# Optimization experiments

Measured on AMD Instinct MI355X. Metric: run time of the kernel, lower is better.

The kernel has to match this reference:

```python
import jax, jax.numpy as jnp
import numpy as np

VOCAB = 50000
B, T, D_OUT = 32, 512, 256
E_DIMS = (300, 300, 200)


def setup_inputs() -> dict:
    key = jax.random.key(0)
    ks = jax.random.split(key, 8)
    ids = jax.random.randint(ks[0], (B, T), 0, VOCAB)
    E0 = jax.random.normal(ks[1], (VOCAB, E_DIMS[0]), dtype=jnp.float32)
    E1 = jax.random.normal(ks[2], (VOCAB, E_DIMS[1]), dtype=jnp.float32)
    E2 = jax.random.normal(ks[3], (VOCAB, E_DIMS[2]), dtype=jnp.float32)
    # Glorot-ish scaled projection weights
    W0 = jax.random.normal(ks[4], (E_DIMS[0], D_OUT), dtype=jnp.float32) / np.sqrt(E_DIMS[0])
    W1 = jax.random.normal(ks[5], (E_DIMS[1], D_OUT), dtype=jnp.float32) / np.sqrt(E_DIMS[1])
    W2 = jax.random.normal(ks[6], (E_DIMS[2], D_OUT), dtype=jnp.float32) / np.sqrt(E_DIMS[2])
    Wa = jax.random.normal(ks[7], (D_OUT, 1), dtype=jnp.float32) / np.sqrt(D_OUT)
    return {
        "ids": ids,
        "E0": E0, "E1": E1, "E2": E2,
        "W0": W0, "b0": jnp.zeros((D_OUT,), jnp.float32),
        "W1": W1, "b1": jnp.zeros((D_OUT,), jnp.float32),
        "W2": W2, "b2": jnp.zeros((D_OUT,), jnp.float32),
        "Wa": Wa, "ba": jnp.zeros((1,), jnp.float32),
    }


def reference(ids, E0, E1, E2, W0, b0, W1, b1, W2, b2, Wa, ba):
    # Per-source embedding gather + Dense projection -> [B, T, D_OUT]
    p0 = E0[ids] @ W0 + b0
    p1 = E1[ids] @ W1 + b1
    p2 = E2[ids] @ W2 + b2
    projected = jnp.stack([p0, p1, p2], axis=2)  # [B, T, n_emb, D]
    # Attention Dense(1) over D, softmax over the n_emb axis
    logits = jnp.einsum('btnd,do->btno', projected, Wa) + ba  # [B, T, n, 1]
    alphas = jax.nn.softmax(logits, axis=2)
    # Weighted combine: matmul(projected^T, alphas) then squeeze -> [B, T, D]
    out = jnp.einsum('btnd,btn->btd', projected, alphas[..., 0])
    return out
```

## Files before the change

kernel.cpp:

```cpp
#include <hip/hip_runtime.h>
#include <hip/hip_bf16.h>

typedef __attribute__((ext_vector_type(8))) short short8;
typedef __attribute__((ext_vector_type(4))) float floatx4;
typedef unsigned short ushort_t;
typedef unsigned int uint_t;

#define DOUT   256
#define KPAD   864
#define XPITCH 872
#define TB     32
#define NTOK   16384
#define NPREP_T 27
#define NPREP_U 225

static __device__ inline uint_t pack2bf(float x, float y) {
    __hip_bfloat162 h = __float22bfloat162_rn(make_float2(x, y));
    return *(uint_t*)&h;
}
static __device__ inline ushort_t f2bf(float f) {
    union { float f; uint_t u; } a; a.f = f;
    uint_t u = a.u;
    return (ushort_t)((u + 0x7FFFu + ((u >> 16) & 1u)) >> 16);
}

__global__ __launch_bounds__(256) void k_prep(
    const float* __restrict__ W0, const float* __restrict__ W1,
    const float* __restrict__ W2,
    const float* __restrict__ b0, const float* __restrict__ b1,
    const float* __restrict__ b2,
    const float* __restrict__ Wa, const float* __restrict__ ba,
    float* __restrict__ u, float* __restrict__ lb, ushort_t* __restrict__ Wtf)
{
    __shared__ ushort_t tile[32][258];
    int tid = threadIdx.x;
    if (blockIdx.x < NPREP_T) {
        int kc = blockIdx.x;
        for (int idx = tid; idx < 32 * 64; idx += 256) {
            int kk = idx >> 6, c4 = idx & 63;
            int kp = kc * 32 + kk;
            float4 v = make_float4(0.f, 0.f, 0.f, 0.f);
            const float* src = nullptr;
            if (kp < 320)      { if (kp < 300) src = W0 + kp * DOUT; }
            else if (kp < 640) { int o = kp - 320; if (o < 300) src = W1 + o * DOUT; }
            else               { int o = kp - 640; if (o < 200) src = W2 + o * DOUT; }
            if (src) v = *(const float4*)(src + 4 * c4);
            tile[kk][4 * c4 + 0] = f2bf(v.x);
            tile[kk][4 * c4 + 1] = f2bf(v.y);
            tile[kk][4 * c4 + 2] = f2bf(v.z);
            tile[kk][4 * c4 + 3] = f2bf(v.w);
        }
        __syncthreads();
        int lane = tid & 63;
        int ntg = tid >> 6;
        int kq = (lane >> 4) * 8;
        int nc = lane & 15;
        #pragma unroll
        for (int i = 0; i < 4; ++i) {
            int nt = ntg * 4 + i;
            union { uint4 v; ushort_t s[8]; } p;
            #pragma unroll
            for (int j = 0; j < 8; ++j) p.s[j] = tile[kq + j][nt * 16 + nc];
            *(uint4*)(Wtf + ((size_t)(nt * 27 + kc) * 64 + lane) * 8) = p.v;
        }
    } else {
        int lane = tid & 63;
        int w = tid >> 6;
        int kp = (blockIdx.x - NPREP_T) * 4 + w;
        if (kp > 898) return;
        const float* row = nullptr;
        if (kp < 320)       { if (kp < 300) row = W0 + kp * DOUT; }
        else if (kp < 640)  { int o = kp - 320; if (o < 300) row = W1 + o * DOUT; }
        else if (kp < 864)  { int o = kp - 640; if (o < 200) row = W2 + o * DOUT; }
        else if (kp >= 896) { int n = kp - 896; row = (n == 0) ? b0 : ((n == 1) ? b1 : b2); }
        float acc = 0.f;
        if (row) {
            #pragma unroll
            for (int j = lane; j < DOUT; j += 64)
                acc += row[j] * Wa[j];
        }
        for (int off = 32; off > 0; off >>= 1) acc += __shfl_down(acc, off);
        if (lane == 0) {
            if (kp < 896) u[kp] = acc;
            else          lb[kp - 896] = acc + ba[0];
        }
    }
}

__global__ __launch_bounds__(512, 4) void k_main(
    const int* __restrict__ ids,
    const float* __restrict__ E0, const float* __restrict__ E1,
    const float* __restrict__ E2,
    const float* __restrict__ b0, const float* __restrict__ b1,
    const float* __restrict__ b2,
    const float* __restrict__ u, const float* __restrict__ lb,
    const ushort_t* __restrict__ Wtf,
    float* __restrict__ out)
{
    __shared__ __align__(16) ushort_t Xs[TB][XPITCH];
    __shared__ float alphaS[TB][4];

    int tid = threadIdx.x;
    int tok0 = blockIdx.x * TB;

    int trow = tid >> 4, sub = tid & 15;
    int id = ids[tok0 + trow];
    uint2* Xd2 = (uint2*)&Xs[trow][0];
    const float4* p0 = (const float4*)E0 + (size_t)id * 75;
    const float4* p1 = (const float4*)E1 + (size_t)id * 75;
    const float4* p2 = (const float4*)E2 + (size_t)id * 50;
    float4 f4z = make_float4(0.f, 0.f, 0.f, 0.f);

    float4 g[14];
    g[0] = p0[sub];      g[1] = p0[sub + 16];
    g[2] = p0[sub + 32]; g[3] = p0[sub + 48];
    g[4] = (sub < 11) ? p0[sub + 64] : f4z;
    g[5] = p1[sub];      g[6] = p1[sub + 16];
    g[7] = p1[sub + 32]; g[8] = p1[sub + 48];
    g[9] = (sub < 11) ? p1[sub + 64] : f4z;
    g[10] = p2[sub];      g[11] = p2[sub + 16];
    g[12] = p2[sub + 32];
    g[13] = (sub < 2) ? p2[sub + 48] : f4z;
    __builtin_amdgcn_sched_barrier(0);

    float l0 = 0.f, l1 = 0.f, l2 = 0.f;
    #pragma unroll
    for (int j = 0; j < 5; ++j) {
        float4 t = g[j], uu = *(const float4*)(u + 4 * (sub + 16 * j));
        l0 += t.x * uu.x + t.y * uu.y + t.z * uu.z + t.w * uu.w;
    }
    #pragma unroll
    for (int j = 0; j < 5; ++j) {
        float4 t = g[5 + j], uu = *(const float4*)(u + 320 + 4 * (sub + 16 * j));
        l1 += t.x * uu.x + t.y * uu.y + t.z * uu.z + t.w * uu.w;
    }
    #pragma unroll
    for (int j = 0; j < 4; ++j) {
        float4 t = g[10 + j], uu = *(const float4*)(u + 640 + 4 * (sub + 16 * j));
        l2 += t.x * uu.x + t.y * uu.y + t.z * uu.z + t.w * uu.w;
    }
    #pragma unroll
    for (int m = 1; m < 16; m <<= 1) {
        l0 += __shfl_xor(l0, m);
        l1 += __shfl_xor(l1, m);
        l2 += __shfl_xor(l2, m);
    }
    l0 += lb[0]; l1 += lb[1]; l2 += lb[2];
    float mx = fmaxf(l0, fmaxf(l1, l2));
    float e0 = __expf(l0 - mx), e1 = __expf(l1 - mx), e2 = __expf(l2 - mx);
    float inv = 1.f / (e0 + e1 + e2);
    float a0 = e0 * inv, a1 = e1 * inv, a2 = e2 * inv;
    if (sub == 0) { alphaS[trow][0] = a0; alphaS[trow][1] = a1; alphaS[trow][2] = a2; }

    #pragma unroll
    for (int j = 0; j < 5; ++j) {
        float4 t = g[j];
        Xd2[sub + 16 * j] = make_uint2(pack2bf(a0 * t.x, a0 * t.y), pack2bf(a0 * t.z, a0 * t.w));
    }
    #pragma unroll
    for (int j = 0; j < 5; ++j) {
        float4 t = g[5 + j];
        Xd2[80 + sub + 16 * j] = make_uint2(pack2bf(a1 * t.x, a1 * t.y), pack2bf(a1 * t.z, a1 * t.w));
    }
    #pragma unroll
    for (int j = 0; j < 3; ++j) {
        float4 t = g[10 + j];
        Xd2[160 + sub + 16 * j] = make_uint2(pack2bf(a2 * t.x, a2 * t.y), pack2bf(a2 * t.z, a2 * t.w));
    }
    if (sub < 2) {
        float4 t = g[13];
        Xd2[160 + 48 + sub] = make_uint2(pack2bf(a2 * t.x, a2 * t.y), pack2bf(a2 * t.z, a2 * t.w));
    }
    uint2 z2 = make_uint2(0u, 0u);
    for (int i = 75 + sub;  i < 80;  i += 16) Xd2[i] = z2;
    for (int i = 155 + sub; i < 160; i += 16) Xd2[i] = z2;
    for (int i = 210 + sub; i < 218; i += 16) Xd2[i] = z2;
    __syncthreads();

    int lane = tid & 63;
    int w = tid >> 6;
    int mrow = lane & 15;
    int kg8 = (lane >> 4) * 8;

    const ushort_t* bq0 = Wtf + ((size_t)((2 * w + 0) * 27) * 64 + lane) * 8;
    const ushort_t* bq1 = Wtf + ((size_t)((2 * w + 1) * 27) * 64 + lane) * 8;

    floatx4 acc[2][2];
    {
        floatx4 z = {0.f, 0.f, 0.f, 0.f};
        acc[0][0] = z; acc[0][1] = z; acc[1][0] = z; acc[1][1] = z;
    }

    #pragma unroll
    for (int kc = 0; kc < 27; ++kc) {
        short8 av0 = *(const short8*)&Xs[mrow][kc * 32 + kg8];
        short8 av1 = *(const short8*)&Xs[16 + mrow][kc * 32 + kg8];
        short8 bv0 = *(const short8*)(bq0 + kc * 512);
        short8 bv1 = *(const short8*)(bq1 + kc * 512);
        acc[0][0] = __builtin_amdgcn_mfma_f32_16x16x32_bf16(av0, bv0, acc[0][0], 0, 0, 0);
        acc[1][0] = __builtin_amdgcn_mfma_f32_16x16x32_bf16(av1, bv0, acc[1][0], 0, 0, 0);
        acc[0][1] = __builtin_amdgcn_mfma_f32_16x16x32_bf16(av0, bv1, acc[0][1], 0, 0, 0);
        acc[1][1] = __builtin_amdgcn_mfma_f32_16x16x32_bf16(av1, bv1, acc[1][1], 0, 0, 0);
    }

    float bb0[2], bb1[2], bb2[2];
    #pragma unroll
    for (int nt = 0; nt < 2; ++nt) {
        int n = (2 * w + nt) * 16 + mrow;
        bb0[nt] = b0[n]; bb1[nt] = b1[n]; bb2[nt] = b2[n];
    }
    #pragma unroll
    for (int mt = 0; mt < 2; ++mt) {
        #pragma unroll
        for (int r = 0; r < 4; ++r) {
            int tok = mt * 16 + (lane >> 4) * 4 + r;
            float t0 = alphaS[tok][0], t1 = alphaS[tok][1], t2 = alphaS[tok][2];
            size_t rowoff = (size_t)(tok0 + tok) * DOUT;
            #pragma unroll
            for (int nt = 0; nt < 2; ++nt) {
                int n = (2 * w + nt) * 16 + mrow;
                out[rowoff + n] = acc[mt][nt][r] + t0 * bb0[nt] + t1 * bb1[nt] + t2 * bb2[nt];
            }
        }
    }
}

extern "C" void kernel_launch(void* const* d_in, const int* in_sizes, int n_in,
                              void* d_out, int out_size, void* d_ws, size_t ws_size,
                              hipStream_t stream) {
    const int*   ids = (const int*)d_in[0];
    const float* E0  = (const float*)d_in[1];
    const float* E1  = (const float*)d_in[2];
    const float* E2  = (const float*)d_in[3];
    const float* W0  = (const float*)d_in[4];
    const float* b0  = (const float*)d_in[5];
    const float* W1  = (const float*)d_in[6];
    const float* b1  = (const float*)d_in[7];
    const float* W2  = (const float*)d_in[8];
    const float* b2  = (const float*)d_in[9];
    const float* Wa  = (const float*)d_in[10];
    const float* ba  = (const float*)d_in[11];

    float* u      = (float*)d_ws;
    float* lb     = u + 896;
    ushort_t* Wtf = (ushort_t*)((char*)d_ws + 4096);

    k_prep<<<NPREP_T + NPREP_U, 256, 0, stream>>>(W0, W1, W2, b0, b1, b2, Wa, ba,
                                                  u, lb, Wtf);
    k_main<<<NTOK / TB, 512, 0, stream>>>(ids, E0, E1, E2, b0, b1, b2, u, lb, Wtf,
                                          (float*)d_out);
}
```

Before: 191.2 us.

## Split fused gather-GEMM into separate gather and LDS-tiled GEMM kernels

Splits the fused kernel in two. The first kernel gathers the embedding rows, applies the softmax weights and writes a bf16 X matrix to workspace. It also folds the alphas into extra K columns so the bias terms become part of the GEMM. The second kernel is a 64x128 tiled MFMA GEMM that loads A and B tiles into LDS with global_load_lds. This is meant to improve reuse of the weight matrix and the MFMA tiling, which the old version limited to 32 tokens per block reading B straight from global memory. The cost is an extra global round-trip of the X matrix (about 29MB of bf16), one more kernel launch, and a GEMM loop with no double-buffering that syncs twice per K step.

```diff
diff --git a/kernel.cpp b/kernel.cpp
--- a/kernel.cpp
+++ b/kernel.cpp
@@ -7,21 +7,24 @@
 typedef unsigned int uint_t;
 
 #define DOUT   256
-#define KPAD   864
-#define XPITCH 872
-#define TB     32
+#define KEXT   896
 #define NTOK   16384
-#define NPREP_T 27
-#define NPREP_U 225
-
-static __device__ inline uint_t pack2bf(float x, float y) {
-    __hip_bfloat162 h = __float22bfloat162_rn(make_float2(x, y));
-    return *(uint_t*)&h;
-}
+#define WG_BLKS 56
+#define U_BLKS  225
+
 static __device__ inline ushort_t f2bf(float f) {
     union { float f; uint_t u; } a; a.f = f;
     uint_t u = a.u;
     return (ushort_t)((u + 0x7FFFu + ((u >> 16) & 1u)) >> 16);
+}
+static __device__ inline uint_t pack2bf(float x, float y) {
+    __hip_bfloat162 h = __float22bfloat162_rn(make_float2(x, y));
+    return *(uint_t*)&h;
+}
+static __device__ inline void gload_lds16(const void* g, void* l) {
+    __builtin_amdgcn_global_load_lds(
+        (const __attribute__((address_space(1))) void*)g,
+        (__attribute__((address_space(3))) void*)l, 16, 0, 0);
 }
 
 __global__ __launch_bounds__(256) void k_prep(
@@ -30,43 +33,41 @@
     const float* __restrict__ b0, const float* __restrict__ b1,
     const float* __restrict__ b2,
     const float* __restrict__ Wa, const float* __restrict__ ba,
-    float* __restrict__ u, float* __restrict__ lb, ushort_t* __restrict__ Wtf)
+    float* __restrict__ u, float* __restrict__ lb, ushort_t* __restrict__ Wg)
 {
-    __shared__ ushort_t tile[32][258];
     int tid = threadIdx.x;
-    if (blockIdx.x < NPREP_T) {
-        int kc = blockIdx.x;
-        for (int idx = tid; idx < 32 * 64; idx += 256) {
-            int kk = idx >> 6, c4 = idx & 63;
+    if (blockIdx.x < WG_BLKS) {
+        __shared__ ushort_t tile[32][130];
+        int nblk = blockIdx.x / 28, kc = blockIdx.x % 28;
+        for (int idx = tid; idx < 1024; idx += 256) {
+            int kk = idx >> 5, c4 = idx & 31;
             int kp = kc * 32 + kk;
+            int col = nblk * 128 + c4 * 4;
             float4 v = make_float4(0.f, 0.f, 0.f, 0.f);
-            const float* src = nullptr;
-            if (kp < 320)      { if (kp < 300) src = W0 + kp * DOUT; }
-            else if (kp < 640) { int o = kp - 320; if (o < 300) src = W1 + o * DOUT; }
-            else               { int o = kp - 640; if (o < 200) src = W2 + o * DOUT; }
-            if (src) v = *(const float4*)(src + 4 * c4);
-            tile[kk][4 * c4 + 0] = f2bf(v.x);
-            tile[kk][4 * c4 + 1] = f2bf(v.y);
-            tile[kk][4 * c4 + 2] = f2bf(v.z);
-            tile[kk][4 * c4 + 3] = f2bf(v.w);
+            if (kp < 300)                    v = *(const float4*)(W0 + (size_t)kp * DOUT + col);
+            else if (kp >= 320 && kp < 620)  v = *(const float4*)(W1 + (size_t)(kp - 320) * DOUT + col);
+            else if (kp >= 640 && kp < 840)  v = *(const float4*)(W2 + (size_t)(kp - 640) * DOUT + col);
+            else if (kp == 864)              v = *(const float4*)(b0 + col);
+            else if (kp == 865)              v = *(const float4*)(b1 + col);
+            else if (kp == 866)              v = *(const float4*)(b2 + col);
+            tile[kk][c4 * 4 + 0] = f2bf(v.x);
+            tile[kk][c4 * 4 + 1] = f2bf(v.y);
+            tile[kk][c4 * 4 + 2] = f2bf(v.z);
+            tile[kk][c4 * 4 + 3] = f2bf(v.w);
         }
         __syncthreads();
-        int lane = tid & 63;
-        int ntg = tid >> 6;
-        int kq = (lane >> 4) * 8;
-        int nc = lane & 15;
-        #pragma unroll
-        for (int i = 0; i < 4; ++i) {
-            int nt = ntg * 4 + i;
+        for (int t = tid; t < 512; t += 256) {
+            int i = t >> 6, l = t & 63;
+            int nl = i * 16 + (l >> 2), kj = (l & 3) * 8;
             union { uint4 v; ushort_t s[8]; } p;
             #pragma unroll
-            for (int j = 0; j < 8; ++j) p.s[j] = tile[kq + j][nt * 16 + nc];
-            *(uint4*)(Wtf + ((size_t)(nt * 27 + kc) * 64 + lane) * 8) = p.v;
+            for (int j = 0; j < 8; ++j) p.s[j] = tile[kj + j][nl];
+            *(uint4*)(Wg + (((size_t)(nblk * 28 + kc) * 8 + i) * 64 + l) * 8) = p.v;
         }
     } else {
         int lane = tid & 63;
         int w = tid >> 6;
-        int kp = (blockIdx.x - NPREP_T) * 4 + w;
+        int kp = (blockIdx.x - WG_BLKS) * 4 + w;
         if (kp > 898) return;
         const float* row = nullptr;
         if (kp < 320)       { if (kp < 300) row = W0 + kp * DOUT; }
@@ -87,60 +88,51 @@
     }
 }
 
-__global__ __launch_bounds__(512, 4) void k_main(
+__global__ __launch_bounds__(256, 8) void k_gather(
     const int* __restrict__ ids,
     const float* __restrict__ E0, const float* __restrict__ E1,
     const float* __restrict__ E2,
-    const float* __restrict__ b0, const float* __restrict__ b1,
-    const float* __restrict__ b2,
     const float* __restrict__ u, const float* __restrict__ lb,
-    const ushort_t* __restrict__ Wtf,
-    float* __restrict__ out)
+    ushort_t* __restrict__ Xg)
 {
-    __shared__ __align__(16) ushort_t Xs[TB][XPITCH];
-    __shared__ float alphaS[TB][4];
-
     int tid = threadIdx.x;
-    int tok0 = blockIdx.x * TB;
-
-    int trow = tid >> 4, sub = tid & 15;
-    int id = ids[tok0 + trow];
-    uint2* Xd2 = (uint2*)&Xs[trow][0];
+    int trow = tid >> 5, sub = tid & 31;
+    int tok = blockIdx.x * 8 + trow;
+    int id = ids[tok];
     const float4* p0 = (const float4*)E0 + (size_t)id * 75;
     const float4* p1 = (const float4*)E1 + (size_t)id * 75;
     const float4* p2 = (const float4*)E2 + (size_t)id * 50;
-    float4 f4z = make_float4(0.f, 0.f, 0.f, 0.f);
-
-    float4 g[14];
-    g[0] = p0[sub];      g[1] = p0[sub + 16];
-    g[2] = p0[sub + 32]; g[3] = p0[sub + 48];
-    g[4] = (sub < 11) ? p0[sub + 64] : f4z;
-    g[5] = p1[sub];      g[6] = p1[sub + 16];
-    g[7] = p1[sub + 32]; g[8] = p1[sub + 48];
-    g[9] = (sub < 11) ? p1[sub + 64] : f4z;
-    g[10] = p2[sub];      g[11] = p2[sub + 16];
-    g[12] = p2[sub + 32];
-    g[13] = (sub < 2) ? p2[sub + 48] : f4z;
-    __builtin_amdgcn_sched_barrier(0);
-
-    float l0 = 0.f, l1 = 0.f, l2 = 0.f;
+    float4 z4 = make_float4(0.f, 0.f, 0.f, 0.f);
+
+    float4 g0 = p0[sub], g1 = p0[32 + sub], g2 = (sub < 11) ? p0[64 + sub] : z4;
+    float4 g3 = p1[sub], g4 = p1[32 + sub], g5 = (sub < 11) ? p1[64 + sub] : z4;
+    float4 g6 = p2[sub], g7 = (sub < 18) ? p2[32 + sub] : z4;
+
+    float l0, l1, l2;
+    {
+        float4 ua = *(const float4*)(u + 4 * sub);
+        float4 ub = *(const float4*)(u + 128 + 4 * sub);
+        float4 uc = *(const float4*)(u + 256 + 4 * sub);
+        l0 = g0.x * ua.x + g0.y * ua.y + g0.z * ua.z + g0.w * ua.w
+           + g1.x * ub.x + g1.y * ub.y + g1.z * ub.z + g1.w * ub.w
+           + g2.x * uc.x + g2.y * uc.y + g2.z * uc.z + g2.w * uc.w;
+    }
+    {
+        float4 ua = *(const float4*)(u + 320 + 4 * sub);
+        float4 ub = *(const float4*)(u + 448 + 4 * sub);
+        float4 uc = *(const float4*)(u + 576 + 4 * sub);
+        l1 = g3.x * ua.x + g3.y * ua.y + g3.z * ua.z + g3.w * ua.w
+           + g4.x * ub.x + g4.y * ub.y + g4.z * ub.z + g4.w * ub.w
+           + g5.x * uc.x + g5.y * uc.y + g5.z * uc.z + g5.w * uc.w;
+    }
+    {
+        float4 ua = *(const float4*)(u + 640 + 4 * sub);
+        float4 ub = *(const float4*)(u + 768 + 4 * sub);
+        l2 = g6.x * ua.x + g6.y * ua.y + g6.z * ua.z + g6.w * ua.w
+           + g7.x * ub.x + g7.y * ub.y + g7.z * ub.z + g7.w * ub.w;
+    }
     #pragma unroll
-    for (int j = 0; j < 5; ++j) {
-        float4 t = g[j], uu = *(const float4*)(u + 4 * (sub + 16 * j));
-        l0 += t.x * uu.x + t.y * uu.y + t.z * uu.z + t.w * uu.w;
-    }
-    #pragma unroll
-    for (int j = 0; j < 5; ++j) {
-        float4 t = g[5 + j], uu = *(const float4*)(u + 320 + 4 * (sub + 16 * j));
-        l1 += t.x * uu.x + t.y * uu.y + t.z * uu.z + t.w * uu.w;
-    }
-    #pragma unroll
-    for (int j = 0; j < 4; ++j) {
-        float4 t = g[10 + j], uu = *(const float4*)(u + 640 + 4 * (sub + 16 * j));
-        l2 += t.x * uu.x + t.y * uu.y + t.z * uu.z + t.w * uu.w;
-    }
-    #pragma unroll
-    for (int m = 1; m < 16; m <<= 1) {
+    for (int m = 1; m < 32; m <<= 1) {
         l0 += __shfl_xor(l0, m);
         l1 += __shfl_xor(l1, m);
         l2 += __shfl_xor(l2, m);
@@ -150,77 +142,82 @@
     float e0 = __expf(l0 - mx), e1 = __expf(l1 - mx), e2 = __expf(l2 - mx);
     float inv = 1.f / (e0 + e1 + e2);
     float a0 = e0 * inv, a1 = e1 * inv, a2 = e2 * inv;
-    if (sub == 0) { alphaS[trow][0] = a0; alphaS[trow][1] = a1; alphaS[trow][2] = a2; }
-
+
+    uint2* Xrow = (uint2*)(Xg + (size_t)tok * KEXT);
+    #define PK(G, A) make_uint2(pack2bf((A) * (G).x, (A) * (G).y), pack2bf((A) * (G).z, (A) * (G).w))
+    Xrow[sub]       = PK(g0, a0);
+    Xrow[32 + sub]  = PK(g1, a0);
+    if (sub < 16) Xrow[64 + sub] = PK(g2, a0);
+    Xrow[80 + sub]  = PK(g3, a1);
+    Xrow[112 + sub] = PK(g4, a1);
+    if (sub < 16) Xrow[144 + sub] = PK(g5, a1);
+    Xrow[160 + sub] = PK(g6, a2);
+    uint2 v;
+    if (sub < 18)       v = PK(g7, a2);
+    else if (sub == 24) v = make_uint2(pack2bf(a0, a1), pack2bf(a2, 0.f));
+    else                v = make_uint2(0u, 0u);
+    Xrow[192 + sub] = v;
+    #undef PK
+}
+
+__global__ __launch_bounds__(256, 4) void k_gemm(
+    const ushort_t* __restrict__ Xg, const ushort_t* __restrict__ Wg,
+    float* __restrict__ out)
+{
+    __shared__ __align__(16) ushort_t As[64 * 32];
+    __shared__ __align__(16) ushort_t Bs[128 * 32];
+
+    int tid = threadIdx.x, lane = tid & 63, w = tid >> 6;
+    int mblk = (int)blockIdx.x >> 1, nblk = (int)blockIdx.x & 1;
+    int tok0 = mblk * 64;
+
+    int ra = w * 16 + (lane >> 2);
+    const ushort_t* gA = Xg + (size_t)(tok0 + ra) * KEXT + (lane & 3) * 8;
+    ushort_t* lA  = As + w * 512 + lane * 8;
+    ushort_t* lB0 = Bs + w * 512 + lane * 8;
+    ushort_t* lB1 = Bs + (w + 4) * 512 + lane * 8;
+
+    int m_off = (w & 1) * 32, n_off = (w >> 1) * 64;
+    floatx4 acc[2][4];
     #pragma unroll
-    for (int j = 0; j < 5; ++j) {
-        float4 t = g[j];
-        Xd2[sub + 16 * j] = make_uint2(pack2bf(a0 * t.x, a0 * t.y), pack2bf(a0 * t.z, a0 * t.w));
-    }
-    #pragma unroll
-    for (int j = 0; j < 5; ++j) {
-        float4 t = g[5 + j];
-        Xd2[80 + sub + 16 * j] = make_uint2(pack2bf(a1 * t.x, a1 * t.y), pack2bf(a1 * t.z, a1 * t.w));
-    }
-    #pragma unroll
-    for (int j = 0; j < 3; ++j) {
-        float4 t = g[10 + j];
-        Xd2[160 + sub + 16 * j] = make_uint2(pack2bf(a2 * t.x, a2 * t.y), pack2bf(a2 * t.z, a2 * t.w));
-    }
-    if (sub < 2) {
-        float4 t = g[13];
-        Xd2[160 + 48 + sub] = make_uint2(pack2bf(a2 * t.x, a2 * t.y), pack2bf(a2 * t.z, a2 * t.w));
-    }
-    uint2 z2 = make_uint2(0u, 0u);
-    for (int i = 75 + sub;  i < 80;  i += 16) Xd2[i] = z2;
-    for (int i = 155 + sub; i < 160; i += 16) Xd2[i] = z2;
-    for (int i = 210 + sub; i < 218; i += 16) Xd2[i] = z2;
-    __syncthreads();
-
-    int lane = tid & 63;
-    int w = tid >> 6;
-    int mrow = lane & 15;
-    int kg8 = (lane >> 4) * 8;
-
-    const ushort_t* bq0 = Wtf + ((size_t)((2 * w + 0) * 27) * 64 + lane) * 8;
-    const ushort_t* bq1 = Wtf + ((size_t)((2 * w + 1) * 27) * 64 + lane) * 8;
-
-    floatx4 acc[2][2];
-    {
-        floatx4 z = {0.f, 0.f, 0.f, 0.f};
-        acc[0][0] = z; acc[0][1] = z; acc[1][0] = z; acc[1][1] = z;
-    }
-
-    #pragma unroll
-    for (int kc = 0; kc < 27; ++kc) {
-        short8 av0 = *(const short8*)&Xs[mrow][kc * 32 + kg8];
-        short8 av1 = *(const short8*)&Xs[16 + mrow][kc * 32 + kg8];
-        short8 bv0 = *(const short8*)(bq0 + kc * 512);
-        short8 bv1 = *(const short8*)(bq1 + kc * 512);
-        acc[0][0] = __builtin_amdgcn_mfma_f32_16x16x32_bf16(av0, bv0, acc[0][0], 0, 0, 0);
-        acc[1][0] = __builtin_amdgcn_mfma_f32_16x16x32_bf16(av1, bv0, acc[1][0], 0, 0, 0);
-        acc[0][1] = __builtin_amdgcn_mfma_f32_16x16x32_bf16(av0, bv1, acc[0][1], 0, 0, 0);
-        acc[1][1] = __builtin_amdgcn_mfma_f32_16x16x32_bf16(av1, bv1, acc[1][1], 0, 0, 0);
-    }
-
-    float bb0[2], bb1[2], bb2[2];
-    #pragma unroll
-    for (int nt = 0; nt < 2; ++nt) {
-        int n = (2 * w + nt) * 16 + mrow;
-        bb0[nt] = b0[n]; bb1[nt] = b1[n]; bb2[nt] = b2[n];
-    }
+    for (int mt = 0; mt < 2; ++mt)
+        #pragma unroll
+        for (int nt = 0; nt < 4; ++nt) {
+            floatx4 z = {0.f, 0.f, 0.f, 0.f};
+            acc[mt][nt] = z;
+        }
+
+    for (int kc = 0; kc < 28; ++kc) {
+        gload_lds16(gA + kc * 32, lA);
+        const ushort_t* gBb = Wg + (((size_t)(nblk * 28 + kc) * 8) * 64 + lane) * 8;
+        gload_lds16(gBb + (size_t)w * 512, lB0);
+        gload_lds16(gBb + (size_t)(w + 4) * 512, lB1);
+        __syncthreads();
+
+        short8 aF[2], bF[4];
+        #pragma unroll
+        for (int mt = 0; mt < 2; ++mt)
+            aF[mt] = *(const short8*)(As + (m_off + mt * 16 + (lane & 15)) * 32 + (lane >> 4) * 8);
+        #pragma unroll
+        for (int nt = 0; nt < 4; ++nt)
+            bF[nt] = *(const short8*)(Bs + (n_off + nt * 16 + (lane & 15)) * 32 + (lane >> 4) * 8);
+        #pragma unroll
+        for (int mt = 0; mt < 2; ++mt)
+            #pragma unroll
+            for (int nt = 0; nt < 4; ++nt)
+                acc[mt][nt] = __builtin_amdgcn_mfma_f32_16x16x32_bf16(aF[mt], bF[nt], acc[mt][nt], 0, 0, 0);
+        __syncthreads();
+    }
+
     #pragma unroll
     for (int mt = 0; mt < 2; ++mt) {
         #pragma unroll
         for (int r = 0; r < 4; ++r) {
-            int tok = mt * 16 + (lane >> 4) * 4 + r;
-            float t0 = alphaS[tok][0], t1 = alphaS[tok][1], t2 = alphaS[tok][2];
-            size_t rowoff = (size_t)(tok0 + tok) * DOUT;
-            #pragma unroll
-            for (int nt = 0; nt < 2; ++nt) {
-                int n = (2 * w + nt) * 16 + mrow;
-                out[rowoff + n] = acc[mt][nt][r] + t0 * bb0[nt] + t1 * bb1[nt] + t2 * bb2[nt];
-            }
+            int tok = tok0 + m_off + mt * 16 + (lane >> 4) * 4 + r;
+            size_t rowoff = (size_t)tok * DOUT + nblk * 128;
+            #pragma unroll
+            for (int nt = 0; nt < 4; ++nt)
+                out[rowoff + n_off + nt * 16 + (lane & 15)] = acc[mt][nt][r];
         }
     }
 }
@@ -243,10 +240,11 @@
 
     float* u      = (float*)d_ws;
     float* lb     = u + 896;
-    ushort_t* Wtf = (ushort_t*)((char*)d_ws + 4096);
-
-    k_prep<<<NPREP_T + NPREP_U, 256, 0, stream>>>(W0, W1, W2, b0, b1, b2, Wa, ba,
-                                                  u, lb, Wtf);
-    k_main<<<NTOK / TB, 512, 0, stream>>>(ids, E0, E1, E2, b0, b1, b2, u, lb, Wtf,
-                                          (float*)d_out);
-}
+    ushort_t* Wg  = (ushort_t*)((char*)d_ws + 4096);
+    ushort_t* Xg  = (ushort_t*)((char*)d_ws + (512 << 10));
+
+    k_prep<<<WG_BLKS + U_BLKS, 256, 0, stream>>>(W0, W1, W2, b0, b1, b2, Wa, ba,
+                                                 u, lb, Wg);
+    k_gather<<<NTOK / 8, 256, 0, stream>>>(ids, E0, E1, E2, u, lb, Xg);
+    k_gemm<<<(NTOK / 64) * 2, 256, 0, stream>>>(Xg, Wg, (float*)d_out);
+}
```

New measurement: 195.6 us. 1.02x slower.
